# Optimization experiments

Measured on AMD Instinct MI355X. Metric: run time of the kernel, lower is better.

The kernel has to match this reference:

```python
import jax, jax.numpy as jnp
import numpy as np

ACT_SCALE = 1.0 / 12.0
BATCH = 2_097_152
HIDDEN = 32


def _xavier(key, shape):
    fan_out, fan_in = shape
    std = (2.0 / (fan_in + fan_out)) ** 0.5
    return jax.random.normal(key, shape, dtype=jnp.float32) * std


def setup_inputs() -> dict:
    key = jax.random.key(0)
    ks = jax.random.split(key, 12)
    return {
        "eps_flat": jax.random.normal(ks[0], (BATCH, 3), dtype=jnp.float32) * 0.1,
        "B_first_w": _xavier(ks[1], (HIDDEN, 2)),
        "B_first_b": jax.random.normal(ks[2], (HIDDEN,), dtype=jnp.float32) * 0.05,
        "raw_A_0": jax.random.normal(ks[3], (HIDDEN, HIDDEN), dtype=jnp.float32) * 0.1,
        "raw_A_1": jax.random.normal(ks[4], (HIDDEN, HIDDEN), dtype=jnp.float32) * 0.1,
        "Bs_w_0": _xavier(ks[5], (HIDDEN, 2)),
        "Bs_b_0": jax.random.normal(ks[6], (HIDDEN,), dtype=jnp.float32) * 0.05,
        "Bs_w_1": _xavier(ks[7], (HIDDEN, 2)),
        "Bs_b_1": jax.random.normal(ks[8], (HIDDEN,), dtype=jnp.float32) * 0.05,
        "raw_A_out": jax.random.normal(ks[9], (1, HIDDEN), dtype=jnp.float32) * 0.1,
        "B_out_w": _xavier(ks[10], (1, 2)),
        "B_out_b": jax.random.normal(ks[11], (1,), dtype=jnp.float32) * 0.05,
    }


def reference(eps_flat, B_first_w, B_first_b, raw_A_0, raw_A_1,
              Bs_w_0, Bs_b_0, Bs_w_1, Bs_b_1, raw_A_out, B_out_w, B_out_b):
    sp = jax.nn.softplus

    def forward_W(z0):
        # z0: (n, 2) -> W: (n, 1). Dropout p=0 -> identity.
        z = sp(z0 @ B_first_w.T + B_first_b)
        for rawA, Bw, Bb in ((raw_A_0, Bs_w_0, Bs_b_0), (raw_A_1, Bs_w_1, Bs_b_1)):
            z = ACT_SCALE * sp(z @ sp(rawA).T) ** 2 + sp(z0 @ Bw.T + Bb)
        return z @ sp(raw_A_out).T + z0 @ B_out_w.T + B_out_b

    e11, e22, e12 = eps_flat[:, 0], eps_flat[:, 1], eps_flat[:, 2]
    I1 = e11 + e22
    I2 = e11 ** 2 + 2.0 * e12 ** 2 + e22 ** 2
    z0 = jnp.stack([I1, I2], axis=-1)  # (B, 2)

    W_sum = lambda z: forward_W(z).sum()
    grads = jax.grad(W_sum)(z0)                       # (B, 2) per-sample dW/dz0
    z0_ref = jnp.zeros((1, 2), dtype=eps_flat.dtype)
    dWdI1_ref = jax.grad(W_sum)(z0_ref)[0, 0]         # scalar reference correction

    dW_dI1 = grads[:, 0] - dWdI1_ref
    dW_dI2 = grads[:, 1]
    s11 = dW_dI1 + 2.0 * e11 * dW_dI2
    s22 = dW_dI1 + 2.0 * e22 * dW_dI2
    s12 = 2.0 * e12 * dW_dI2
    return jnp.stack([s11, s22, s12], axis=-1)
```

## Files before the change

### kernel.cpp

```cpp
#include <hip/hip_runtime.h>

typedef __attribute__((ext_vector_type(8)))  short s8b;
typedef __attribute__((ext_vector_type(16))) float f32x16;
typedef __attribute__((ext_vector_type(4)))  uint  uint4v;
typedef __attribute__((ext_vector_type(2)))  float float2v;
typedef __attribute__((ext_vector_type(4)))  float float4v;
typedef uint __attribute__((may_alias)) uint_ma;

static constexpr int   kBatch    = 2097152;
static constexpr float kActScale = 1.0f / 12.0f;
static constexpr float kAct2     = 1.0f / 6.0f;

__device__ float g_tab[40];
__device__ __attribute__((aligned(16))) ushort g_wt[4][2][2][64][8];
__device__ __attribute__((aligned(16))) ushort g_pt[3][64][8];

__device__ __forceinline__ float rcp_f(float x) { return __fdividef(1.0f, x); }
__device__ __forceinline__ float sp_only(float x) {
    float e = __expf(-fabsf(x));
    return fmaxf(x, 0.0f) + __logf(1.0f + e);
}
__device__ __forceinline__ float sig_only(float x) {
    float e = __expf(-fabsf(x));
    float r = rcp_f(1.0f + e);
    return (x >= 0.0f) ? r : e * r;
}
__device__ __forceinline__ float sp_sig(float x, float& sig) {
    float e  = __expf(-fabsf(x));
    float oe = 1.0f + e;
    float r  = rcp_f(oe);
    sig = (x >= 0.0f) ? r : e * r;
    return fmaxf(x, 0.0f) + __logf(oe);
}

__device__ __forceinline__ float log1p_e(float e) {
    return e * fmaf(e, fmaf(e, fmaf(e, fmaf(e, 0.03215845f, -0.13606275f),
                                    0.28947478f), -0.49190896f), 0.99949556f);
}
__device__ __forceinline__ float rcp12(float u) {
    float r = fmaf(u, -0.5f, 1.4571068f);
    r = r * fmaf(-u, r, 2.0f);
    r = r * fmaf(-u, r, 2.0f);
    return r;
}
__device__ __forceinline__ float sp_sig_p(float x, float& sig) {
    float e = __expf(-fabsf(x));
    float r = rcp12(1.0f + e);
    sig = (x >= 0.0f) ? r : e * r;
    return fmaxf(x, 0.0f) + log1p_e(e);
}
__device__ __forceinline__ float sp_sig_pos(float x, float& sig) {
    float e = __expf(-x);
    sig = rcp12(1.0f + e);
    return x + log1p_e(e);
}
__device__ __forceinline__ float sig_only_p(float x) {
    float e = __expf(-fabsf(x));
    float r = rcp12(1.0f + e);
    return (x >= 0.0f) ? r : e * r;
}

__device__ __forceinline__ uint  bf16u(float x) {
    uint u = __float_as_uint(x);
    return (u + 0x7FFFu + ((u >> 16) & 1u)) >> 16;
}
__device__ __forceinline__ float bf16f(uint h) { return __uint_as_float(h << 16); }
__device__ __forceinline__ uint cvt_pk_bf16(float lo, float hi) {
    uint r;
    asm("v_cvt_pk_bf16_f32 %0, %1, %2" : "=v"(r) : "v"(lo), "v"(hi));
    return r;
}
__device__ __forceinline__ void pswap(uint& a, uint& b) {
    asm("v_permlane32_swap_b32 %0, %1" : "+v"(a), "+v"(b));
}

__global__ __launch_bounds__(256) void icnn_prep(
    const float* __restrict__ rawA0, const float* __restrict__ rawA1,
    const float* __restrict__ rawAout,
    const float* __restrict__ W1,  const float* __restrict__ b1,
    const float* __restrict__ Wc0, const float* __restrict__ bc0,
    const float* __restrict__ Wc1, const float* __restrict__ bc1,
    const float* __restrict__ wout)
{
    __shared__ float sA0[1024], sA1[1024], sAout[32];
    const int t = threadIdx.x;
    for (int k = t; k < 1024; k += 256) sA0[k] = sp_only(rawA0[k]);
    for (int k = t; k < 1024; k += 256) sA1[k] = sp_only(rawA1[k]);
    if (t < 32) { float v = sp_only(rawAout[t]); sAout[t] = v; g_tab[t] = v; }
    __syncthreads();

    for (int k = t; k < 8192; k += 256) {
        int m = k >> 11, r = k & 2047;
        int hl = r >> 10, c = (r >> 9) & 1, l = (r >> 3) & 63, b = r & 7;
        int row = l & 31, j = 16 * c + 8 * (l >> 5) + b;
        float v;
        if      (m == 0) v = sA0[row * 32 + j];
        else if (m == 1) v = sA1[row * 32 + j];
        else if (m == 2) v = sA1[j * 32 + row];
        else             v = sA0[j * 32 + row];
        uint hi = bf16u(v);
        g_wt[m][hl][c][l][b] = (ushort)(hl == 0 ? hi : bf16u(v - bf16f(hi)));
    }

    for (int k = t; k < 1536; k += 256) {
        int m = k >> 9, r = k & 511, l = r >> 3, b = r & 7;
        int unit = l & 31, half = l >> 5;
        ushort v = 0;
        if (half == 0) {
            const float* Wm = (m == 0) ? W1 : ((m == 1) ? Wc0 : Wc1);
            const float* Bm = (m == 0) ? b1 : ((m == 1) ? bc0 : bc1);
            float w1 = Wm[2 * unit], w2 = Wm[2 * unit + 1], bb = Bm[unit];
            uint h;
            switch (b) {
                case 0: v = (ushort)bf16u(w1); break;
                case 1: h = bf16u(w1); v = (ushort)bf16u(w1 - bf16f(h)); break;
                case 2: v = (ushort)bf16u(w2); break;
                case 3: h = bf16u(w2); v = (ushort)bf16u(w2 - bf16f(h)); break;
                case 4: v = (ushort)bf16u(bb); break;
                case 5: h = bf16u(bb); v = (ushort)bf16u(bb - bf16f(h)); break;
                default: v = 0;
            }
        }
        g_pt[m][l][b] = v;
    }

    if (t < 32) {
        const int i = t;
        float sa, sc0v;
        float zi = sp_sig(b1[i], sa);
        float u = 0.0f;
        for (int j = 0; j < 32; j++) u = fmaf(sA0[i * 32 + j], __shfl(zi, j, 64), u);
        float su; float t0 = sp_sig(u, su);
        float d0 = kAct2 * t0 * su;
        float spc = sp_sig(bc0[i], sc0v);
        float zn = fmaf(kActScale * t0, t0, spc);
        float u1 = 0.0f;
        for (int j = 0; j < 32; j++) u1 = fmaf(sA1[i * 32 + j], __shfl(zn, j, 64), u1);
        float su1; float t1 = sp_sig(u1, su1);
        float d1 = sAout[i] * kAct2 * t1 * su1;
        float contrib = Wc1[2 * i] * sAout[i] * sig_only(bc1[i]);
        float g = 0.0f;
        for (int j = 0; j < 32; j++) g = fmaf(sA1[j * 32 + i], __shfl(d1, j, 64), g);
        contrib = fmaf(Wc0[2 * i], g * sc0v, contrib);
        float gu0 = g * d0;
        float ga = 0.0f;
        for (int j = 0; j < 32; j++) ga = fmaf(sA0[j * 32 + i], __shfl(gu0, j, 64), ga);
        ga *= sa;
        contrib = fmaf(W1[2 * i], ga, contrib);
        for (int off = 16; off >= 1; off >>= 1)
            contrib += __shfl_down(contrib, off, 32);
        if (i == 0) g_tab[32] = wout[0] + contrib;
    }
}

__device__ __forceinline__ s8b ldwt(int m, int hl, int c, int lane) {
    const uint_ma* p = (const uint_ma*)&g_wt[m][hl][c][lane][0];
    uint4v q; q.x = p[0]; q.y = p[1]; q.z = p[2]; q.w = p[3];
    return __builtin_bit_cast(s8b, q);
}
__device__ __forceinline__ s8b ldpt(int m, int lane) {
    const uint_ma* p = (const uint_ma*)&g_pt[m][lane][0];
    uint4v q; q.x = p[0]; q.y = p[1]; q.z = p[2]; q.w = p[3];
    return __builtin_bit_cast(s8b, q);
}

#define OFF(e) (((e) & 3) + 8 * ((e) >> 2))

#define SWAPJ(PZ, FA, FB) { \
    uint s0 = PZ[0], s1 = PZ[1], s2 = PZ[2], s3 = PZ[3]; \
    uint s4 = PZ[4], s5 = PZ[5], s6 = PZ[6], s7 = PZ[7]; \
    pswap(s0, s2); pswap(s1, s3); pswap(s4, s6); pswap(s5, s7); \
    uint4v qa, qb; \
    qa.x = s0; qa.y = s1; qa.z = s2; qa.w = s3; \
    qb.x = s4; qb.y = s5; qb.z = s6; qb.w = s7; \
    FA = __builtin_bit_cast(s8b, qa); FB = __builtin_bit_cast(s8b, qb); }

#define MM(m, BA, BB, ACC) { \
    ACC = __builtin_amdgcn_mfma_f32_32x32x16_bf16(ldwt(m, 0, 0, lane), BA, ACC, 0, 0, 0); \
    ACC = __builtin_amdgcn_mfma_f32_32x32x16_bf16(ldwt(m, 0, 1, lane), BB, ACC, 0, 0, 0); \
    ACC = __builtin_amdgcn_mfma_f32_32x32x16_bf16(ldwt(m, 1, 0, lane), BA, ACC, 0, 0, 0); \
    ACC = __builtin_amdgcn_mfma_f32_32x32x16_bf16(ldwt(m, 1, 1, lane), BB, ACC, 0, 0, 0); }

__global__ __launch_bounds__(256) void icnn_main(
    const float* __restrict__ eps,
    const float* __restrict__ W1,  const float* __restrict__ b1,
    const float* __restrict__ Wc0, const float* __restrict__ bc0,
    const float* __restrict__ Wc1, const float* __restrict__ bc1,
    const float* __restrict__ wout,
    float* __restrict__ out)
{
    const int tid  = threadIdx.x;
    const int lane = tid & 63, wib = tid >> 6;
    const bool hb_ = lane >= 32;
    const int  hB  = hb_ ? 1 : 0;
    const int  rowl = lane & 31;
    const long rowg = ((long)blockIdx.x * 4 + wib) * 32 + rowl;

    const float e11 = eps[rowg * 3 + 0];
    const float e22 = eps[rowg * 3 + 1];
    const float e12 = eps[rowg * 3 + 2];
    const float x1 = e11 + e22;
    const float x2 = e11 * e11 + 2.0f * e12 * e12 + e22 * e22;

    const float wout0 = wout[0], wout1 = wout[1];
    const float cref  = g_tab[32];
    const char* W1c  = (const char*)W1;
    const char* Wc0c = (const char*)Wc0;
    const char* Wc1c = (const char*)Wc1;
    const char* aoc  = (const char*)&g_tab[0];

    float g0p = 0.0f, gqp = 0.0f;

    uint x1h = bf16u(x1);
    uint x1l = bf16u(x1 - bf16f(x1h));
    uint x2h = bf16u(x2);
    uint x2l = bf16u(x2 - bf16f(x2h));
    uint4v bq;
    bq.x = hb_ ? 0u : (x1h | (x1l << 16));
    bq.y = hb_ ? 0u : (x2h | (x2l << 16));
    bq.z = hb_ ? 0u : 0x3F803F80u;
    bq.w = 0u;
    s8b bx = __builtin_bit_cast(s8b, bq);
    f32x16 zzz = {};
    f32x16 pa  = __builtin_amdgcn_mfma_f32_32x32x16_bf16(ldpt(0, lane), bx, zzz, 0, 0, 0);
    f32x16 pc0 = __builtin_amdgcn_mfma_f32_32x32x16_bf16(ldpt(1, lane), bx, zzz, 0, 0, 0);
    f32x16 pc1 = __builtin_amdgcn_mfma_f32_32x32x16_bf16(ldpt(2, lane), bx, zzz, 0, 0, 0);

    uint pz[8], psa[8];
    #pragma unroll
    for (int q = 0; q < 8; ++q) {
        const int e = 2 * q;
        float s0, s1;
        float z0 = sp_sig_p(pa[e],     s0);
        float z1 = sp_sig_p(pa[e + 1], s1);
        pz[q]  = cvt_pk_bf16(z0, z1);
        psa[q] = cvt_pk_bf16(s0, s1);
    }
    s8b fA, fB;
    SWAPJ(pz, fA, fB)

    f32x16 acc = {};
    MM(0, fA, fB, acc)

    uint pd0[8], psc[8];
    #pragma unroll
    for (int q = 0; q < 8; ++q) {
        const int e = 2 * q;
        float su;  float t  = sp_sig_pos(acc[e], su);
        float su2; float t2 = sp_sig_pos(acc[e + 1], su2);
        float sc0, sc1;
        float spc0 = sp_sig_p(pc0[e],     sc0);
        float spc1 = sp_sig_p(pc0[e + 1], sc1);
        psc[q] = cvt_pk_bf16(sc0, sc1);
        pd0[q] = cvt_pk_bf16(kAct2 * t * su, kAct2 * t2 * su2);
        pz[q]  = cvt_pk_bf16(fmaf(kActScale * t, t, spc0),
                             fmaf(kActScale * t2, t2, spc1));
    }
    SWAPJ(pz, fA, fB)

    f32x16 acc1 = {};
    MM(1, fA, fB, acc1)

    uint pdd[8];
    #pragma unroll
    for (int q = 0; q < 8; ++q) {
        const int e = 2 * q, off = OFF(e);
        const float4v wc = *(const float4v*)(Wc1c + 32 * hB + 8 * off);
        const float2v ao = *(const float2v*)(aoc  + 16 * hB + 4 * off);
        float wA = ao.x * sig_only_p(pc1[e]);
        float wB = ao.y * sig_only_p(pc1[e + 1]);
        g0p = fmaf(wc.x, wA, g0p); gqp = fmaf(wc.y, wA, gqp);
        g0p = fmaf(wc.z, wB, g0p); gqp = fmaf(wc.w, wB, gqp);
        float su;  float t  = sp_sig_pos(acc1[e], su);
        float su2; float t2 = sp_sig_pos(acc1[e + 1], su2);
        pdd[q] = cvt_pk_bf16(ao.x * kAct2 * t * su, ao.y * kAct2 * t2 * su2);
    }
    SWAPJ(pdd, fA, fB)

    f32x16 acc2 = {};
    MM(2, fA, fB, acc2)

    uint pgg[8];
    #pragma unroll
    for (int q = 0; q < 8; ++q) {
        const int e = 2 * q, off = OFF(e);
        const float4v wc = *(const float4v*)(Wc0c + 32 * hB + 8 * off);
        float tA = acc2[e]     * bf16f(psc[q] & 0xFFFFu);
        float tB = acc2[e + 1] * bf16f(psc[q] >> 16);
        g0p = fmaf(wc.x, tA, g0p); gqp = fmaf(wc.y, tA, gqp);
        g0p = fmaf(wc.z, tB, g0p); gqp = fmaf(wc.w, tB, gqp);
        pgg[q] = cvt_pk_bf16(acc2[e] * bf16f(pd0[q] & 0xFFFFu),
                             acc2[e + 1] * bf16f(pd0[q] >> 16));
    }
    SWAPJ(pgg, fA, fB)

    f32x16 acc3 = {};
    MM(3, fA, fB, acc3)

    #pragma unroll
    for (int q = 0; q < 8; ++q) {
        const int e = 2 * q, off = OFF(e);
        const float4v w4 = *(const float4v*)(W1c + 32 * hB + 8 * off);
        float gA = acc3[e]     * bf16f(psa[q] & 0xFFFFu);
        float gB = acc3[e + 1] * bf16f(psa[q] >> 16);
        g0p = fmaf(w4.x, gA, g0p); gqp = fmaf(w4.y, gA, gqp);
        g0p = fmaf(w4.z, gB, g0p); gqp = fmaf(w4.w, gB, gqp);
    }

    uint ga_ = __float_as_uint(g0p), gb_ = ga_;
    pswap(ga_, gb_);
    float g0o = __uint_as_float(hb_ ? ga_ : gb_);
    uint qa_ = __float_as_uint(gqp), qb_ = qa_;
    pswap(qa_, qb_);
    float gqo = __uint_as_float(hb_ ? qa_ : qb_);

    float g0f = wout0 + g0p + g0o;
    float gqf = wout1 + gqp + gqo;
    const float dI1 = g0f - cref;
    const float dI2 = gqf;
    if (!hb_) {
        out[rowg * 3 + 0] = fmaf(2.0f * e11, dI2, dI1);
        out[rowg * 3 + 1] = fmaf(2.0f * e22, dI2, dI1);
        out[rowg * 3 + 2] = 2.0f * e12 * dI2;
    }
}

extern "C" void kernel_launch(void* const* d_in, const int* in_sizes, int n_in,
                              void* d_out, int out_size, void* d_ws, size_t ws_size,
                              hipStream_t stream)
{
    (void)in_sizes; (void)n_in; (void)out_size; (void)d_ws; (void)ws_size;
    const float* eps    = (const float*)d_in[0];
    const float* W1     = (const float*)d_in[1];
    const float* b1     = (const float*)d_in[2];
    const float* rawA0  = (const float*)d_in[3];
    const float* rawA1  = (const float*)d_in[4];
    const float* Wc0    = (const float*)d_in[5];
    const float* bc0    = (const float*)d_in[6];
    const float* Wc1    = (const float*)d_in[7];
    const float* bc1    = (const float*)d_in[8];
    const float* rawAout= (const float*)d_in[9];
    const float* wout   = (const float*)d_in[10];
    float* out = (float*)d_out;

    icnn_prep<<<1, 256, 0, stream>>>(rawA0, rawA1, rawAout, W1, b1, Wc0, bc0, Wc1, bc1, wout);
    icnn_main<<<kBatch / 128, 256, 0, stream>>>(eps, W1, b1, Wc0, bc0, Wc1, bc1, wout, out);
}
```

Before: 192.0 us.

## Add cross split-bf16 terms to preactivation MFMA and interleave projection MFMAs

The preactivation MFMA K-slots are rearranged so the hi/lo bf16 splits of the weights pair with both hi and lo parts of the inputs. This adds cross terms such as w_hi*x_lo and w_lo*x_hi for more accurate first-layer preactivations at no extra MFMA cost. The pc0 and pc1 projection MFMAs are moved next to the matmuls that first need them, which can shorten register live ranges and overlap MFMA with VALU work. Vector float4/float2 loads are replaced by scalar pointer loads, which may change how the loads are issued.

```diff
diff --git a/kernel.cpp b/kernel.cpp
--- a/kernel.cpp
+++ b/kernel.cpp
@@ -3,8 +3,6 @@
 typedef __attribute__((ext_vector_type(8)))  short s8b;
 typedef __attribute__((ext_vector_type(16))) float f32x16;
 typedef __attribute__((ext_vector_type(4)))  uint  uint4v;
-typedef __attribute__((ext_vector_type(2)))  float float2v;
-typedef __attribute__((ext_vector_type(4)))  float float4v;
 typedef uint __attribute__((may_alias)) uint_ma;
 
 static constexpr int   kBatch    = 2097152;
@@ -113,12 +111,13 @@
             uint h;
             switch (b) {
                 case 0: v = (ushort)bf16u(w1); break;
-                case 1: h = bf16u(w1); v = (ushort)bf16u(w1 - bf16f(h)); break;
-                case 2: v = (ushort)bf16u(w2); break;
-                case 3: h = bf16u(w2); v = (ushort)bf16u(w2 - bf16f(h)); break;
-                case 4: v = (ushort)bf16u(bb); break;
-                case 5: h = bf16u(bb); v = (ushort)bf16u(bb - bf16f(h)); break;
-                default: v = 0;
+                case 1: v = (ushort)bf16u(w1); break;
+                case 2: h = bf16u(w1); v = (ushort)bf16u(w1 - bf16f(h)); break;
+                case 3: v = (ushort)bf16u(w2); break;
+                case 4: v = (ushort)bf16u(w2); break;
+                case 5: h = bf16u(w2); v = (ushort)bf16u(w2 - bf16f(h)); break;
+                case 6: v = (ushort)bf16u(bb); break;
+                case 7: h = bf16u(bb); v = (ushort)bf16u(bb - bf16f(h)); break;
             }
         }
         g_pt[m][l][b] = v;
@@ -217,15 +216,13 @@
     uint x2l = bf16u(x2 - bf16f(x2h));
     uint4v bq;
     bq.x = hb_ ? 0u : (x1h | (x1l << 16));
-    bq.y = hb_ ? 0u : (x2h | (x2l << 16));
-    bq.z = hb_ ? 0u : 0x3F803F80u;
-    bq.w = 0u;
+    bq.y = hb_ ? 0u : (x1h | (x2h << 16));
+    bq.z = hb_ ? 0u : (x2l | (x2h << 16));
+    bq.w = hb_ ? 0u : 0x3F803F80u;
     s8b bx = __builtin_bit_cast(s8b, bq);
-    f32x16 zzz = {};
-    f32x16 pa  = __builtin_amdgcn_mfma_f32_32x32x16_bf16(ldpt(0, lane), bx, zzz, 0, 0, 0);
-    f32x16 pc0 = __builtin_amdgcn_mfma_f32_32x32x16_bf16(ldpt(1, lane), bx, zzz, 0, 0, 0);
-    f32x16 pc1 = __builtin_amdgcn_mfma_f32_32x32x16_bf16(ldpt(2, lane), bx, zzz, 0, 0, 0);
-
+    const f32x16 zzz = {};
+
+    f32x16 pa = __builtin_amdgcn_mfma_f32_32x32x16_bf16(ldpt(0, lane), bx, zzz, 0, 0, 0);
     uint pz[8], psa[8];
     #pragma unroll
     for (int q = 0; q < 8; ++q) {
@@ -239,6 +236,7 @@
     s8b fA, fB;
     SWAPJ(pz, fA, fB)
 
+    f32x16 pc0 = __builtin_amdgcn_mfma_f32_32x32x16_bf16(ldpt(1, lane), bx, zzz, 0, 0, 0);
     f32x16 acc = {};
     MM(0, fA, fB, acc)
 
@@ -258,6 +256,7 @@
     }
     SWAPJ(pz, fA, fB)
 
+    f32x16 pc1 = __builtin_amdgcn_mfma_f32_32x32x16_bf16(ldpt(2, lane), bx, zzz, 0, 0, 0);
     f32x16 acc1 = {};
     MM(1, fA, fB, acc1)
 
@@ -265,15 +264,15 @@
     #pragma unroll
     for (int q = 0; q < 8; ++q) {
         const int e = 2 * q, off = OFF(e);
-        const float4v wc = *(const float4v*)(Wc1c + 32 * hB + 8 * off);
-        const float2v ao = *(const float2v*)(aoc  + 16 * hB + 4 * off);
-        float wA = ao.x * sig_only_p(pc1[e]);
-        float wB = ao.y * sig_only_p(pc1[e + 1]);
-        g0p = fmaf(wc.x, wA, g0p); gqp = fmaf(wc.y, wA, gqp);
-        g0p = fmaf(wc.z, wB, g0p); gqp = fmaf(wc.w, wB, gqp);
+        const float* wc4 = (const float*)(Wc1c + 32 * hB + 8 * off);
+        const float* ao2 = (const float*)(aoc  + 16 * hB + 4 * off);
+        float wA = ao2[0] * sig_only_p(pc1[e]);
+        float wB = ao2[1] * sig_only_p(pc1[e + 1]);
+        g0p = fmaf(wc4[0], wA, g0p); gqp = fmaf(wc4[1], wA, gqp);
+        g0p = fmaf(wc4[2], wB, g0p); gqp = fmaf(wc4[3], wB, gqp);
         float su;  float t  = sp_sig_pos(acc1[e], su);
         float su2; float t2 = sp_sig_pos(acc1[e + 1], su2);
-        pdd[q] = cvt_pk_bf16(ao.x * kAct2 * t * su, ao.y * kAct2 * t2 * su2);
+        pdd[q] = cvt_pk_bf16(ao2[0] * kAct2 * t * su, ao2[1] * kAct2 * t2 * su2);
     }
     SWAPJ(pdd, fA, fB)
 
@@ -284,11 +283,11 @@
     #pragma unroll
     for (int q = 0; q < 8; ++q) {
         const int e = 2 * q, off = OFF(e);
-        const float4v wc = *(const float4v*)(Wc0c + 32 * hB + 8 * off);
+        const float* wc4 = (const float*)(Wc0c + 32 * hB + 8 * off);
         float tA = acc2[e]     * bf16f(psc[q] & 0xFFFFu);
         float tB = acc2[e + 1] * bf16f(psc[q] >> 16);
-        g0p = fmaf(wc.x, tA, g0p); gqp = fmaf(wc.y, tA, gqp);
-        g0p = fmaf(wc.z, tB, g0p); gqp = fmaf(wc.w, tB, gqp);
+        g0p = fmaf(wc4[0], tA, g0p); gqp = fmaf(wc4[1], tA, gqp);
+        g0p = fmaf(wc4[2], tB, g0p); gqp = fmaf(wc4[3], tB, gqp);
         pgg[q] = cvt_pk_bf16(acc2[e] * bf16f(pd0[q] & 0xFFFFu),
                              acc2[e + 1] * bf16f(pd0[q] >> 16));
     }
@@ -300,11 +299,11 @@
     #pragma unroll
     for (int q = 0; q < 8; ++q) {
         const int e = 2 * q, off = OFF(e);
-        const float4v w4 = *(const float4v*)(W1c + 32 * hB + 8 * off);
+        const float* w4 = (const float*)(W1c + 32 * hB + 8 * off);
         float gA = acc3[e]     * bf16f(psa[q] & 0xFFFFu);
         float gB = acc3[e + 1] * bf16f(psa[q] >> 16);
-        g0p = fmaf(w4.x, gA, g0p); gqp = fmaf(w4.y, gA, gqp);
-        g0p = fmaf(w4.z, gB, g0p); gqp = fmaf(w4.w, gB, gqp);
+        g0p = fmaf(w4[0], gA, g0p); gqp = fmaf(w4[1], gA, gqp);
+        g0p = fmaf(w4[2], gB, g0p); gqp = fmaf(w4[3], gB, gqp);
     }
 
     uint ga_ = __float_as_uint(g0p), gb_ = ga_;
```

After: 189.0 us. No clear change (-1.5%).
